# Kernel tuning notes

Measured on AMD Instinct MI355X. Metric: run time of the kernel, lower is better.

## Reference

```python
import jax, jax.numpy as jnp
import numpy as np

HEADS = 16
THETA = 10000.0


def _rope(x, pos):
    # x: [b, h, s, d_k], pos: [b, s] int
    d_k = x.shape[-1]
    inv_freq = 1.0 / (THETA ** (jnp.arange(0, d_k, 2, dtype=jnp.float32) / d_k))  # [d_k/2]
    ang = pos[..., None].astype(jnp.float32) * inv_freq                           # [b, s, d_k/2]
    cos = jnp.cos(ang)[:, None, :, :]  # [b, 1, s, d_k/2] broadcast over heads
    sin = jnp.sin(ang)[:, None, :, :]
    x_even = x[..., 0::2]
    x_odd = x[..., 1::2]
    r_even = x_even * cos - x_odd * sin
    r_odd = x_even * sin + x_odd * cos
    return jnp.stack([r_even, r_odd], axis=-1).reshape(x.shape)


def setup_inputs() -> dict:
    key = jax.random.key(0)
    ks = jax.random.split(key, 5)
    B, S, D = 4, 2048, 1024
    std = float(np.sqrt(1.0 / D))
    def w(k):
        return jnp.clip(jax.random.normal(k, (D, D), jnp.float32) * std, -3 * std, 3 * std)
    return {
        "x": jax.random.normal(ks[0], (B, S, D), jnp.float32),
        "token_positions": jnp.broadcast_to(jnp.arange(S, dtype=jnp.int32), (B, S)),
        "wq": w(ks[1]),
        "wk": w(ks[2]),
        "wv": w(ks[3]),
        "wo": w(ks[4]),
    }


def reference(x, token_positions, wq, wk, wv, wo):
    B, S, D = x.shape
    h = HEADS
    dk = D // h
    # Projections: einsum 'hd d, ... s d -> ... s hd' == x @ W.T
    def proj(w):
        return jnp.einsum('bsd,kd->bsk', x, w).reshape(B, S, h, dk).transpose(0, 2, 1, 3)
    q = _rope(proj(wq), token_positions)  # [b,h,s,dk]
    k = _rope(proj(wk), token_positions)
    v = proj(wv)
    scores = jnp.einsum('bhqd,bhkd->bhqk', q, k) / np.sqrt(dk).astype(np.float32)
    causal = jnp.tril(jnp.ones((S, S), bool))
    scores = jnp.where(causal, scores, jnp.finfo(scores.dtype).min)
    attn = jax.nn.softmax(scores, axis=-1)
    out = jnp.einsum('bhqk,bhkd->bhqd', attn, v)        # [b,h,s,dk]
    out = out.transpose(0, 2, 1, 3).reshape(B, S, D)    # [b,s,h*dk]
    return jnp.einsum('bsv,dv->bsd', out, wo)
```

## Files before the change

### kernel.cpp

```cpp
#include <hip/hip_runtime.h>
#include <hip/hip_bf16.h>
#include <stdint.h>

typedef __bf16 bf16;
typedef __bf16 bf16x4 __attribute__((ext_vector_type(4)));
typedef __bf16 bf16x8 __attribute__((ext_vector_type(8)));
typedef float f32x4 __attribute__((ext_vector_type(4)));
typedef float f32x16 __attribute__((ext_vector_type(16)));

#define GLDS16(g, l) __builtin_amdgcn_global_load_lds( \
    (const __attribute__((address_space(1))) void*)(g), \
    (__attribute__((address_space(3))) void*)(l), 16, 0, 0)

static constexpr int S = 2048;

__global__ __launch_bounds__(256) void cvt_all(const float* __restrict__ x,
                                               const float* __restrict__ wq,
                                               const float* __restrict__ wk,
                                               const float* __restrict__ wv,
                                               const float* __restrict__ wo,
                                               bf16* __restrict__ xb,
                                               bf16* __restrict__ wqkvb,
                                               bf16* __restrict__ wob) {
  const int bid = blockIdx.x;
  const float* src;
  bf16* dst;
  int i;
  if (bid < 4096) {
    src = x; dst = xb; i = bid * 256 + threadIdx.x;
  } else {
    int w = (bid - 4096) >> 9;
    i = ((bid - 4096) & 511) * 256 + threadIdx.x;
    src = (w == 0) ? wq : (w == 1) ? wk : (w == 2) ? wv : wo;
    dst = (w == 3) ? wob : wqkvb + (size_t)w * 1048576;
  }
  const float4* p = (const float4*)src + (size_t)i * 2;
  float4 a = p[0], b = p[1];
  bf16x8 o;
  o[0] = (bf16)a.x; o[1] = (bf16)a.y; o[2] = (bf16)a.z; o[3] = (bf16)a.w;
  o[4] = (bf16)b.x; o[5] = (bf16)b.y; o[6] = (bf16)b.z; o[7] = (bf16)b.w;
  *((bf16x8*)dst + i) = o;
}

template <int MODE>
__global__ __launch_bounds__(256, 2) void gemm_k(const bf16* __restrict__ xA,
                                                 const bf16* __restrict__ wB,
                                                 const int* __restrict__ tp,
                                                 bf16* __restrict__ oq,
                                                 bf16* __restrict__ ok,
                                                 bf16* __restrict__ ov,
                                                 float* __restrict__ outf) {
  constexpr int K = 1024;
  __shared__ __align__(16) char lds[65536];
  const int t = threadIdx.x, l = t & 63, wid = t >> 6;
  const int wm = wid >> 1, wn = wid & 1;

  int sel, tA, tB;
  const bf16 *Ap, *Bp;
  const int raw = blockIdx.x;
  if (MODE == 0) {
    int wg = (raw & 7) * 192 + (raw >> 3);
    if (wg < 1024) {
      sel = wg >> 9;
      int r2 = wg & 511;
      tB = r2 >> 6;
      tA = r2 & 63;
      Ap = xA + (size_t)tA * 128 * K;
      Bp = wB + (size_t)(sel * 1024 + tB * 128) * K;
    } else {
      sel = 2;
      int r2 = wg - 1024;
      tA = r2 >> 6;
      tB = r2 & 63;
      Ap = wB + (size_t)(2048 + tA * 128) * K;
      Bp = xA + (size_t)tB * 128 * K;
    }
  } else {
    int wg = (raw & 7) * 64 + (raw >> 3);
    sel = 3;
    tA = wg >> 3; tB = wg & 7;
    Ap = xA + (size_t)tA * 128 * K;
    Bp = wB + (size_t)tB * 128 * K;
  }

  const int lrow = l >> 3;
  const int cswz = ((l & 7) ^ (lrow & 7)) * 8;
  const bf16* aS = Ap + (size_t)(wid * 32 + lrow) * K + cswz;
  const bf16* bS = Bp + (size_t)(wid * 32 + lrow) * K + cswz;

  auto stage = [&](int kt, int buf) {
    char* base = lds + buf * 32768;
#pragma unroll
    for (int g = 0; g < 4; g++)
      GLDS16(aS + (size_t)(8 * g) * K + kt, base + (wid * 32 + 8 * g) * 128);
#pragma unroll
    for (int g = 0; g < 4; g++)
      GLDS16(bS + (size_t)(8 * g) * K + kt,
             base + 16384 + (wid * 32 + 8 * g) * 128);
  };

  int offA[4][2], offB[4][2];
#pragma unroll
  for (int f = 0; f < 4; f++)
#pragma unroll
    for (int kk = 0; kk < 2; kk++) {
      int ra = wm * 64 + f * 16 + (l & 15);
      offA[f][kk] = ra * 128 + (((kk * 4 + (l >> 4)) ^ (ra & 7)) * 16);
      int rb = wn * 64 + f * 16 + (l & 15);
      offB[f][kk] = 16384 + rb * 128 + (((kk * 4 + (l >> 4)) ^ (rb & 7)) * 16);
    }

  f32x4 acc[4][4] = {};

  stage(0, 0);
#pragma unroll 1
  for (int t_ = 0; t_ < 16; ++t_) {
    if (t_ < 15) {
      stage((t_ + 1) * 64, (t_ + 1) & 1);
      asm volatile("s_waitcnt vmcnt(8)" ::: "memory");
    } else {
      asm volatile("s_waitcnt vmcnt(0)" ::: "memory");
    }
    __builtin_amdgcn_s_barrier();
    __builtin_amdgcn_sched_barrier(0);

    const char* base = lds + (t_ & 1) * 32768;
    bf16x8 af[4][2], bg[4][2];
#pragma unroll
    for (int f = 0; f < 4; f++)
#pragma unroll
      for (int kk = 0; kk < 2; kk++) {
        af[f][kk] = *(const bf16x8*)(base + offA[f][kk]);
        bg[f][kk] = *(const bf16x8*)(base + offB[f][kk]);
      }
    __builtin_amdgcn_s_setprio(1);
#pragma unroll
    for (int mi = 0; mi < 4; mi++)
#pragma unroll
      for (int ni = 0; ni < 4; ni++)
#pragma unroll
        for (int kk = 0; kk < 2; kk++)
          acc[mi][ni] = __builtin_amdgcn_mfma_f32_16x16x32_bf16(
              af[mi][kk], bg[ni][kk], acc[mi][ni], 0, 0, 0);
    __builtin_amdgcn_s_setprio(0);
    asm volatile("s_waitcnt lgkmcnt(0)" ::: "memory");
    __builtin_amdgcn_sched_barrier(0);
    __builtin_amdgcn_s_barrier();
  }

  if (MODE == 2) {
    const int rbase = tA * 128 + wm * 64 + (l >> 4) * 4;
    const int cbase = tB * 128 + wn * 64 + (l & 15);
#pragma unroll
    for (int mi = 0; mi < 4; mi++)
#pragma unroll
      for (int ni = 0; ni < 4; ni++)
#pragma unroll
        for (int r = 0; r < 4; r++)
          outf[(size_t)(rbase + mi * 16 + r) * 1024 + cbase + ni * 16] =
              acc[mi][ni][r];
    return;
  }

#pragma unroll
  for (int mi = 0; mi < 4; mi++)
#pragma unroll
    for (int ni = 0; ni < 4; ni++)
#pragma unroll
      for (int r = 0; r < 4; r++) {
        int row = wm * 64 + mi * 16 + (l >> 4) * 4 + r;
        int col = wn * 64 + ni * 16 + (l & 15);
        *(bf16*)(lds + row * 272 + col * 2) = (bf16)acc[mi][ni][r];
      }
  __syncthreads();

#pragma unroll 1
  for (int i = 0; i < 8; ++i) {
    const int id = t + 256 * i;
    const int row = id >> 4, ch = id & 15;
    bf16x8 v8 = *(const bf16x8*)(lds + row * 272 + ch * 16);
    if (sel < 2) {
      const int m = tA * 128 + row;
      const float p = (float)tp[m];
      const int g = ch & 7;
      bf16x8 o;
#pragma unroll
      for (int j = 0; j < 4; j++) {
        float ang = p * exp2f((float)(g * 4 + j) * -0.4152410118609203f);
        float sn, cs;
        sincosf(ang, &sn, &cs);
        float e = (float)v8[2 * j], od = (float)v8[2 * j + 1];
        o[2 * j]     = (bf16)(e * cs - od * sn);
        o[2 * j + 1] = (bf16)(e * sn + od * cs);
      }
      bf16* dst = (sel == 0) ? oq : ok;
      const int h = tB * 2 + (ch >> 3);
      size_t idx = ((size_t)((m >> 11) * 16 + h) << 17) +
                   ((size_t)(m & 2047) << 6) + g * 8;
      *(bf16x8*)(dst + idx) = o;
    } else {
      const int dd = tA * 128 + row;
      const int h = dd >> 6;
      const int s0 = tB * 128 + ch * 8;
      size_t idx = ((size_t)((s0 >> 11) * 16 + h) << 17) +
                   ((size_t)(dd & 63) << 11) + (s0 & 2047);
      *(bf16x8*)(ov + idx) = v8;
    }
  }
}

__global__ __launch_bounds__(512) void attn_k(const bf16* __restrict__ q,
                                              const bf16* __restrict__ k,
                                              const bf16* __restrict__ vt,
                                              bf16* __restrict__ att) {
  __shared__ bf16 Ks[3][4096];
  __shared__ bf16 Vs[3][4096];

  const int t = threadIdx.x, l = t & 63, w = t >> 6;
  const int hi2 = l >> 5, q5 = l & 31;

  const int raw = blockIdx.y * 4 + blockIdx.x;
  const int wg = (raw & 7) * 32 + (raw >> 3);
  const int j_ = wg & 3;
  const int bh = wg >> 2;

  const bf16* qb = q + (size_t)bh * S * 64;
  const bf16* kb = k + (size_t)bh * S * 64;
  const bf16* vb = vt + (size_t)bh * 64 * S;

  const int lrow = l >> 3;
  const int clog = ((l & 7) ^ (lrow & 7)) * 8;

  auto stage = [&](int nt, int b) {
    GLDS16(kb + (size_t)(nt * 64 + w * 8 + lrow) * 64 + clog, &Ks[b][w * 512]);
    GLDS16(vb + (size_t)(w * 8 + lrow) * S + nt * 64 + clog, &Vs[b][w * 512]);
  };

  const int swz = (q5 & 7) << 4;
  int kaddr[4], vaddr[8];
#pragma unroll
  for (int c = 0; c < 4; c++)
    kaddr[c] = q5 * 128 + ((32 * c + 16 * hi2) ^ swz);
#pragma unroll
  for (int m = 0; m < 8; m++)
    vaddr[m] = q5 * 128 + ((16 * m) ^ swz) + 8 * hi2;

  const int b_ = bh >> 4, h_ = bh & 15;
  const char* KsB = (const char*)&Ks[0][0];
  const char* VsB = (const char*)&Vs[0][0];

  for (int pass = 0; pass < 2; ++pass) {
    const int qt = pass ? j_ : 7 - j_;
    const int qrow = qt * 256 + w * 32 + q5;
    bf16x8 qf[4];
#pragma unroll
    for (int c = 0; c < 4; c++) {
      bf16x8 rq = *(const bf16x8*)&qb[(size_t)qrow * 64 + 16 * c + 8 * hi2];
      bf16x8 s_;
#pragma unroll
      for (int j2 = 0; j2 < 8; j2++)
        s_[j2] = (bf16)((float)rq[j2] * 0.18033688011112042f);
      qf[c] = s_;
    }

    f32x16 acc[2] = {};
    float l_r = 0.f;
    const int nkv = 4 * qt + 4;
    const int qmaxw = qt * 256 + w * 32 + 31;

    int cur = 0, nxt = 1, ovr = 2;
    stage(0, 0);
    stage(1, 1);
#pragma unroll 1
    for (int nt = 0; nt < nkv; ++nt) {
      if (nt + 2 < nkv) {
        stage(nt + 2, ovr);
        asm volatile("s_waitcnt vmcnt(4)" ::: "memory");
      } else if (nt + 1 < nkv) {
        asm volatile("s_waitcnt vmcnt(2)" ::: "memory");
      } else {
        asm volatile("s_waitcnt vmcnt(0)" ::: "memory");
      }
      __builtin_amdgcn_s_barrier();
      __builtin_amdgcn_sched_barrier(0);

      const bool live = (64 * nt) <= qmaxw;
      if (live) {
        const int bo = cur * 8192;

        f32x16 sc[2] = {};
        __builtin_amdgcn_s_setprio(1);
#pragma unroll
        for (int c = 0; c < 4; c++) {
#pragma unroll
          for (int T = 0; T < 2; T++) {
            bf16x8 kf = *(const bf16x8*)(KsB + bo + T * 4096 + kaddr[c]);
            sc[T] = __builtin_amdgcn_mfma_f32_32x32x16_bf16(kf, qf[c], sc[T], 0, 0, 0);
          }
        }
        __builtin_amdgcn_s_setprio(0);

        if (64 * nt + 63 > qt * 256 + w * 32) {
#pragma unroll
          for (int T = 0; T < 2; T++)
#pragma unroll
            for (int r = 0; r < 16; r++) {
              int kvg = 64 * nt + 32 * T + (r & 3) + 8 * (r >> 2) + 4 * hi2;
              if (kvg > qrow) sc[T][r] = -1e30f;
            }
        }

        float rs = 0.f;
#pragma unroll
        for (int T = 0; T < 2; T++)
#pragma unroll
          for (int r = 0; r < 16; r++) {
            float pv = __builtin_amdgcn_exp2f(sc[T][r]);
            sc[T][r] = pv;
            rs += pv;
          }
        rs += __shfl_xor(rs, 32);
        l_r += rs;

        bf16x8 pa[4];
#pragma unroll
        for (int c = 0; c < 4; c++)
#pragma unroll
          for (int j2 = 0; j2 < 8; j2++)
            pa[c][j2] = (bf16)sc[c >> 1][8 * (c & 1) + j2];

        __builtin_amdgcn_s_setprio(1);
#pragma unroll
        for (int c = 0; c < 4; c++) {
#pragma unroll
          for (int dt = 0; dt < 2; dt++) {
            bf16x4 v0 = *(const bf16x4*)(VsB + bo + dt * 4096 + vaddr[2 * c]);
            bf16x4 v1 = *(const bf16x4*)(VsB + bo + dt * 4096 + vaddr[2 * c + 1]);
            bf16x8 bv;
#pragma unroll
            for (int j2 = 0; j2 < 4; j2++) { bv[j2] = v0[j2]; bv[4 + j2] = v1[j2]; }
            acc[dt] = __builtin_amdgcn_mfma_f32_32x32x16_bf16(pa[c], bv, acc[dt], 0, 0, 0);
          }
        }
        __builtin_amdgcn_s_setprio(0);
      }

      asm volatile("s_waitcnt lgkmcnt(0)" ::: "memory");
      __builtin_amdgcn_sched_barrier(0);
      __builtin_amdgcn_s_barrier();
      int t3 = cur; cur = nxt; nxt = ovr; ovr = t3;
    }

    float linv = 1.f / l_r;
#pragma unroll
    for (int r = 0; r < 16; r++) {
      int rmap = (r & 3) + 8 * (r >> 2) + 4 * hi2;
      float li = __shfl(linv, rmap);
      int rowq = qt * 256 + w * 32 + rmap;
      size_t rb = ((size_t)(b_ * S + rowq) << 10) + h_ * 64 + q5;
#pragma unroll
      for (int dt = 0; dt < 2; dt++)
        att[rb + 32 * dt] = (bf16)(acc[dt][r] * li);
    }
  }
}

extern "C" void kernel_launch(void* const* d_in, const int* in_sizes, int n_in,
                              void* d_out, int out_size, void* d_ws, size_t ws_size,
                              hipStream_t stream) {
  const float* x  = (const float*)d_in[0];
  const int* tp   = (const int*)d_in[1];
  const float* wq = (const float*)d_in[2];
  const float* wk = (const float*)d_in[3];
  const float* wv = (const float*)d_in[4];
  const float* wo = (const float*)d_in[5];
  float* out = (float*)d_out;

  char* ws = (char*)d_ws;
  const size_t TEN = 16777216;
  bf16* x_bf    = (bf16*)(ws);
  bf16* q_bf    = (bf16*)(ws + TEN);
  bf16* k_bf    = (bf16*)(ws + 2 * TEN);
  bf16* v_bf    = (bf16*)(ws + 3 * TEN);
  bf16* wqkv_bf = (bf16*)(ws + 4 * TEN);
  bf16* wo_bf   = wqkv_bf + 3 * 1048576;
  bf16* att_bf  = x_bf;

  cvt_all<<<6144, 256, 0, stream>>>(x, wq, wk, wv, wo, x_bf, wqkv_bf, wo_bf);

  gemm_k<0><<<1536, 256, 0, stream>>>(x_bf, wqkv_bf, tp, q_bf, k_bf, v_bf,
                                      nullptr);

  dim3 ga(4, 64);
  attn_k<<<ga, 512, 0, stream>>>(q_bf, k_bf, v_bf, att_bf);

  gemm_k<2><<<512, 256, 0, stream>>>(att_bf, wo_bf, nullptr, nullptr, nullptr,
                                     nullptr, out);
}
```

Baseline: 169.5 us.

## Use triple-buffered BK=32 GEMM pipeline with higher occupancy and plain 2D grid

The projection GEMMs now use a K-tile of 32 instead of 64, with three rotating LDS buffers and a prefetch distance of two, so the LDS footprint falls to 48KB and launch bounds rise to 3 blocks per CU. The swizzle and LDS addressing are reworked for 64-byte rows. The aim is better latency hiding from deeper prefetch and more resident waves. The XCD-aware block remapping is replaced with a plain 2D grid, which can hurt L2 locality, and the shorter K step doubles the number of barriers per tile.

```diff
diff --git a/kernel.cpp b/kernel.cpp
--- a/kernel.cpp
+++ b/kernel.cpp
@@ -43,7 +43,7 @@
 }
 
 template <int MODE>
-__global__ __launch_bounds__(256, 2) void gemm_k(const bf16* __restrict__ xA,
+__global__ __launch_bounds__(256, 3) void gemm_k(const bf16* __restrict__ xA,
                                                  const bf16* __restrict__ wB,
                                                  const int* __restrict__ tp,
                                                  bf16* __restrict__ oq,
@@ -51,101 +51,93 @@
                                                  bf16* __restrict__ ov,
                                                  float* __restrict__ outf) {
   constexpr int K = 1024;
-  __shared__ __align__(16) char lds[65536];
+  __shared__ __align__(16) char lds[49152];
   const int t = threadIdx.x, l = t & 63, wid = t >> 6;
   const int wm = wid >> 1, wn = wid & 1;
+  const int bm = blockIdx.x, bn = blockIdx.y;
 
   int sel, tA, tB;
   const bf16 *Ap, *Bp;
-  const int raw = blockIdx.x;
   if (MODE == 0) {
-    int wg = (raw & 7) * 192 + (raw >> 3);
-    if (wg < 1024) {
-      sel = wg >> 9;
-      int r2 = wg & 511;
-      tB = r2 >> 6;
-      tA = r2 & 63;
+    if (bn < 16) {
+      sel = bn >> 3;
+      tA = bm;
+      tB = bn & 7;
       Ap = xA + (size_t)tA * 128 * K;
       Bp = wB + (size_t)(sel * 1024 + tB * 128) * K;
     } else {
       sel = 2;
-      int r2 = wg - 1024;
-      tA = r2 >> 6;
-      tB = r2 & 63;
+      tA = bn - 16;
+      tB = bm;
       Ap = wB + (size_t)(2048 + tA * 128) * K;
       Bp = xA + (size_t)tB * 128 * K;
     }
   } else {
-    int wg = (raw & 7) * 64 + (raw >> 3);
     sel = 3;
-    tA = wg >> 3; tB = wg & 7;
+    tA = bm; tB = bn;
     Ap = xA + (size_t)tA * 128 * K;
     Bp = wB + (size_t)tB * 128 * K;
   }
 
-  const int lrow = l >> 3;
-  const int cswz = ((l & 7) ^ (lrow & 7)) * 8;
-  const bf16* aS = Ap + (size_t)(wid * 32 + lrow) * K + cswz;
-  const bf16* bS = Bp + (size_t)(wid * 32 + lrow) * K + cswz;
-
-  auto stage = [&](int kt, int buf) {
-    char* base = lds + buf * 32768;
-#pragma unroll
-    for (int g = 0; g < 4; g++)
-      GLDS16(aS + (size_t)(8 * g) * K + kt, base + (wid * 32 + 8 * g) * 128);
-#pragma unroll
-    for (int g = 0; g < 4; g++)
-      GLDS16(bS + (size_t)(8 * g) * K + kt,
-             base + 16384 + (wid * 32 + 8 * g) * 128);
+  const int lrow = l >> 2;
+  const int csrc = ((l & 3) ^ ((l >> 3) & 3)) * 8;
+  const bf16* aS = Ap + (size_t)(wid * 32 + lrow) * K + csrc;
+  const bf16* bS = Bp + (size_t)(wid * 32 + lrow) * K + csrc;
+
+  auto stage = [&](int kt, char* base) {
+    GLDS16(aS + kt, base + (wid * 32) * 64);
+    GLDS16(aS + (size_t)16 * K + kt, base + (wid * 32 + 16) * 64);
+    GLDS16(bS + kt, base + 8192 + (wid * 32) * 64);
+    GLDS16(bS + (size_t)16 * K + kt, base + 8192 + (wid * 32 + 16) * 64);
   };
 
-  int offA[4][2], offB[4][2];
-#pragma unroll
-  for (int f = 0; f < 4; f++)
-#pragma unroll
-    for (int kk = 0; kk < 2; kk++) {
-      int ra = wm * 64 + f * 16 + (l & 15);
-      offA[f][kk] = ra * 128 + (((kk * 4 + (l >> 4)) ^ (ra & 7)) * 16);
-      int rb = wn * 64 + f * 16 + (l & 15);
-      offB[f][kk] = 16384 + rb * 128 + (((kk * 4 + (l >> 4)) ^ (rb & 7)) * 16);
-    }
+  int offA[4], offB[4];
+#pragma unroll
+  for (int f = 0; f < 4; f++) {
+    int ra = wm * 64 + f * 16 + (l & 15);
+    offA[f] = ra * 64 + (((l >> 4) ^ ((ra >> 1) & 3)) * 16);
+    int rb = wn * 64 + f * 16 + (l & 15);
+    offB[f] = 8192 + rb * 64 + (((l >> 4) ^ ((rb >> 1) & 3)) * 16);
+  }
 
   f32x4 acc[4][4] = {};
 
-  stage(0, 0);
+  char* cur = lds;
+  char* nxt = lds + 16384;
+  char* ovr = lds + 32768;
+  stage(0, cur);
+  stage(32, nxt);
 #pragma unroll 1
-  for (int t_ = 0; t_ < 16; ++t_) {
-    if (t_ < 15) {
-      stage((t_ + 1) * 64, (t_ + 1) & 1);
+  for (int t_ = 0; t_ < 32; ++t_) {
+    if (t_ + 2 < 32) {
+      stage((t_ + 2) * 32, ovr);
       asm volatile("s_waitcnt vmcnt(8)" ::: "memory");
+    } else if (t_ + 1 < 32) {
+      asm volatile("s_waitcnt vmcnt(4)" ::: "memory");
     } else {
       asm volatile("s_waitcnt vmcnt(0)" ::: "memory");
     }
     __builtin_amdgcn_s_barrier();
     __builtin_amdgcn_sched_barrier(0);
 
-    const char* base = lds + (t_ & 1) * 32768;
-    bf16x8 af[4][2], bg[4][2];
-#pragma unroll
-    for (int f = 0; f < 4; f++)
-#pragma unroll
-      for (int kk = 0; kk < 2; kk++) {
-        af[f][kk] = *(const bf16x8*)(base + offA[f][kk]);
-        bg[f][kk] = *(const bf16x8*)(base + offB[f][kk]);
-      }
+    bf16x8 af[4], bg[4];
+#pragma unroll
+    for (int f = 0; f < 4; f++) {
+      af[f] = *(const bf16x8*)(cur + offA[f]);
+      bg[f] = *(const bf16x8*)(cur + offB[f]);
+    }
     __builtin_amdgcn_s_setprio(1);
 #pragma unroll
     for (int mi = 0; mi < 4; mi++)
 #pragma unroll
       for (int ni = 0; ni < 4; ni++)
-#pragma unroll
-        for (int kk = 0; kk < 2; kk++)
-          acc[mi][ni] = __builtin_amdgcn_mfma_f32_16x16x32_bf16(
-              af[mi][kk], bg[ni][kk], acc[mi][ni], 0, 0, 0);
+        acc[mi][ni] = __builtin_amdgcn_mfma_f32_16x16x32_bf16(
+            af[mi], bg[ni], acc[mi][ni], 0, 0, 0);
     __builtin_amdgcn_s_setprio(0);
     asm volatile("s_waitcnt lgkmcnt(0)" ::: "memory");
     __builtin_amdgcn_sched_barrier(0);
     __builtin_amdgcn_s_barrier();
+    char* tmp = cur; cur = nxt; nxt = ovr; ovr = tmp;
   }
 
   if (MODE == 2) {
@@ -388,12 +380,14 @@
 
   cvt_all<<<6144, 256, 0, stream>>>(x, wq, wk, wv, wo, x_bf, wqkv_bf, wo_bf);
 
-  gemm_k<0><<<1536, 256, 0, stream>>>(x_bf, wqkv_bf, tp, q_bf, k_bf, v_bf,
-                                      nullptr);
+  dim3 gq(64, 24);
+  gemm_k<0><<<gq, 256, 0, stream>>>(x_bf, wqkv_bf, tp, q_bf, k_bf, v_bf,
+                                    nullptr);
 
   dim3 ga(4, 64);
   attn_k<<<ga, 512, 0, stream>>>(q_bf, k_bf, v_bf, att_bf);
 
-  gemm_k<2><<<512, 256, 0, stream>>>(att_bf, wo_bf, nullptr, nullptr, nullptr,
-                                     nullptr, out);
+  dim3 go(64, 8);
+  gemm_k<2><<<go, 256, 0, stream>>>(att_bf, wo_bf, nullptr, nullptr, nullptr,
+                                    nullptr, out);
 }
```

Result: faster. 160.0 us (-5.6%).
